# Kernel optimization log

Hardware: AMD Instinct MI355X
Metric: run time of the kernel (lower is better)

The kernel has to match this reference:

```python
import jax, jax.numpy as jnp
import numpy as np

EPS = 1e-8
N_REFINE = 10
LR_REFINE = 0.1
N_SAMPLES = 12
M_BLEND = 0.3      # self.m
MARGIN = 0.2
TAU = 0.07
USE_INFONCE = True


def safe_norm(x, axis=-1):
    return x / jnp.clip(jnp.linalg.norm(x, axis=axis, keepdims=True), EPS, None)


def setup_inputs() -> dict:
    key = jax.random.key(0)
    k1, k2, k3, k4 = jax.random.split(key, 4)
    K, C, N, H, W = 10, 768, 8, 64, 64
    fg_proto = safe_norm(jax.random.normal(k1, (K, C), jnp.float32))
    bg_proto = safe_norm(jax.random.normal(k2, (K, C), jnp.float32))
    F_map = jax.random.normal(k3, (N, C, H, W), jnp.float32)
    M_map = jax.random.uniform(k4, (N, 1, H, W), jnp.float32)
    return {"fg_proto": fg_proto, "bg_proto": bg_proto, "F_map": F_map, "M_map": M_map}


def _refine(feats, p0):
    """Iterative spherical k-means style refinement.
    feats: [S, C] unit vectors (constants), p0: [K, C] centers.
    Vectorized segment-sum version of the per-cluster torch loop
    (updates within one iteration are independent across k)."""
    K = p0.shape[0]
    ones = jnp.ones((feats.shape[0],), feats.dtype)

    def body(p, it):
        step = LR_REFINE / (1.0 + 0.5 * it)
        assign = jnp.argmax(feats @ p.T, axis=1)                      # [S]
        sums = jax.ops.segment_sum(feats, assign, num_segments=K)    # [K, C]
        cnts = jax.ops.segment_sum(ones, assign, num_segments=K)     # [K]
        mean = sums / jnp.clip(cnts, 1.0, None)[:, None]
        new = safe_norm((1.0 - step) * p + step * mean)
        p = jnp.where((cnts > 0)[:, None], new, p)
        return p, None

    p, _ = jax.lax.scan(body, p0, jnp.arange(N_REFINE, dtype=p0.dtype))
    return p


def reference(fg_proto, bg_proto, F_map, M_map):
    N, C, H, W = F_map.shape
    # mask already at feature resolution -> nearest interpolate is identity
    M_flat = jnp.clip(M_map, 0.0, 1.0).reshape(-1)                   # [N*H*W]
    F_flat = safe_norm(jnp.transpose(F_map, (0, 2, 3, 1)).reshape(-1, C))

    # min cosine distance to any prototype == 1 - max similarity
    dist_fg_min = 1.0 - jnp.max(F_flat @ fg_proto.T, axis=1)
    dist_bg_min = 1.0 - jnp.max(F_flat @ bg_proto.T, axis=1)
    score_fg = jax.lax.stop_gradient(dist_fg_min * M_flat)
    score_bg = jax.lax.stop_gradient(dist_bg_min * (1.0 - M_flat))
    pos_idx = jax.lax.top_k(score_fg, N_SAMPLES)[1]
    neg_idx = jax.lax.top_k(score_bg, N_SAMPLES)[1]

    pos_feats = F_flat[pos_idx]                                       # [12, C]
    neg_feats = F_flat[neg_idx]

    # refinement runs under torch.no_grad on detached copies
    p_fg = _refine(jax.lax.stop_gradient(pos_feats), jax.lax.stop_gradient(fg_proto))
    p_bg = _refine(jax.lax.stop_gradient(neg_feats), jax.lax.stop_gradient(bg_proto))

    # triplet loss
    pos_n = safe_norm(pos_feats)
    neg_n = safe_norm(neg_feats)
    sim_pos = jnp.mean(jnp.max(pos_n @ p_fg.T, axis=1))
    sim_neg = jnp.mean(jnp.max(neg_n @ p_fg.T, axis=1))
    loss = jax.nn.relu(MARGIN + sim_neg - sim_pos)

    if USE_INFONCE:
        pos_sim = pos_n @ p_fg.T / TAU                                # [12, K]
        neg_sim = pos_n @ p_bg.T / TAU                                # [12, K]
        numer = jax.nn.logsumexp(pos_sim, axis=1)
        denom = jax.nn.logsumexp(jnp.concatenate([pos_sim, neg_sim], axis=1), axis=1)
        loss = loss + 0.25 * (-jnp.mean(numer - denom))

    refined_fg = safe_norm((1.0 - M_BLEND) * fg_proto + M_BLEND * p_fg)
    refined_bg = safe_norm((1.0 - M_BLEND) * bg_proto + M_BLEND * p_bg)
    return loss, refined_fg, refined_bg
```

## Files before the change

### kernel.cpp

```cpp
#include <hip/hip_runtime.h>
#include <math.h>

#define KP   10
#define CC   768
#define NB   8
#define HW   4096
#define STOT 32768
#define NS   12
#define NBLK 256

#define WS_CAND  0
#define WS_FEATS 12352
#define WS_PFG   30784
#define WS_PBG   38464

typedef unsigned long long ull;
typedef float f2v __attribute__((ext_vector_type(2)));

__device__ __forceinline__ f2v fma2(f2v a, float b, f2v c) {
#if __has_builtin(__builtin_elementwise_fma)
    f2v bb = b;
    return __builtin_elementwise_fma(a, bb, c);
#else
    f2v r; r.x = fmaf(a.x, b, c.x); r.y = fmaf(a.y, b, c.y); return r;
#endif
}

__device__ __forceinline__ ull pack_key(float v, int idx) {
    unsigned u = __float_as_uint(v);
    u ^= (unsigned)((int)u >> 31) | 0x80000000u;
    return ((ull)u << 32) | (ull)(0xFFFFFFFFu - (unsigned)idx);
}

__global__ __launch_bounds__(1024) void k_scores(const float* __restrict__ fg,
                                                 const float* __restrict__ bg,
                                                 const float* __restrict__ F,
                                                 const float* __restrict__ M,
                                                 ull* __restrict__ cand) {
    __shared__ float pl[20 * CC];
    __shared__ float part[8][64][2][21];
    __shared__ ull kfl[128], kbl[128];

    const int tid  = threadIdx.x;
    const int w    = __builtin_amdgcn_readfirstlane(tid >> 6);
    const int lane = tid & 63;
    const int b    = blockIdx.x;
    const int n    = b >> 5;
    const int hwb  = (b & 31) * 128 + lane * 2;
    const float* fp = F + ((size_t)n * CC) * HW + hwb;
    const int cbase = w * 48;

    f2v fnA[8], fnB[8];
#pragma unroll
    for (int j = 0; j < 8; ++j)
        fnA[j] = __builtin_nontemporal_load((const f2v*)(fp + (size_t)(cbase + j) * HW));
#pragma unroll
    for (int j = 0; j < 8; ++j)
        fnB[j] = __builtin_nontemporal_load((const f2v*)(fp + (size_t)(cbase + 8 + j) * HW));

    for (int i = tid; i < KP * CC; i += 1024) {
        pl[i]           = fg[i];
        pl[KP * CC + i] = bg[i];
    }
    __syncthreads();

    f2v afg[KP], abg[KP], n2;
#pragma unroll
    for (int k = 0; k < KP; ++k) { afg[k] = 0.f; abg[k] = 0.f; }
    n2 = 0.f;

    for (int c0 = 0; c0 < 48; c0 += 8) {
        f2v f[8];
#pragma unroll
        for (int j = 0; j < 8; ++j) { f[j] = fnA[j]; fnA[j] = fnB[j]; }
        if (c0 + 16 < 48) {
#pragma unroll
            for (int j = 0; j < 8; ++j)
                fnB[j] = __builtin_nontemporal_load((const f2v*)(fp + (size_t)(cbase + c0 + 16 + j) * HW));
        }

#pragma unroll
        for (int k = 0; k < KP; ++k) {
            const float4* pq = (const float4*)&pl[k * CC + cbase + c0];
            float4 a = pq[0], c = pq[1];
            f2v acc = afg[k];
            acc = fma2(f[0], a.x, acc); acc = fma2(f[1], a.y, acc);
            acc = fma2(f[2], a.z, acc); acc = fma2(f[3], a.w, acc);
            acc = fma2(f[4], c.x, acc); acc = fma2(f[5], c.y, acc);
            acc = fma2(f[6], c.z, acc); acc = fma2(f[7], c.w, acc);
            afg[k] = acc;
        }
#pragma unroll
        for (int k = 0; k < KP; ++k) {
            const float4* pq = (const float4*)&pl[(KP + k) * CC + cbase + c0];
            float4 a = pq[0], c = pq[1];
            f2v acc = abg[k];
            acc = fma2(f[0], a.x, acc); acc = fma2(f[1], a.y, acc);
            acc = fma2(f[2], a.z, acc); acc = fma2(f[3], a.w, acc);
            acc = fma2(f[4], c.x, acc); acc = fma2(f[5], c.y, acc);
            acc = fma2(f[6], c.z, acc); acc = fma2(f[7], c.w, acc);
            abg[k] = acc;
        }
#pragma unroll
        for (int j = 0; j < 8; ++j) {
#if __has_builtin(__builtin_elementwise_fma)
            n2 = __builtin_elementwise_fma(f[j], f[j], n2);
#else
            n2.x = fmaf(f[j].x, f[j].x, n2.x); n2.y = fmaf(f[j].y, f[j].y, n2.y);
#endif
        }
    }

    if (w >= 8) {
#pragma unroll
        for (int k = 0; k < KP; ++k) {
            part[w - 8][lane][0][k]      = afg[k].x; part[w - 8][lane][1][k]      = afg[k].y;
            part[w - 8][lane][0][10 + k] = abg[k].x; part[w - 8][lane][1][10 + k] = abg[k].y;
        }
        part[w - 8][lane][0][20] = n2.x; part[w - 8][lane][1][20] = n2.y;
    }
    __syncthreads();
    if (w < 8) {
#pragma unroll
        for (int k = 0; k < KP; ++k) {
            part[w][lane][0][k]      += afg[k].x; part[w][lane][1][k]      += afg[k].y;
            part[w][lane][0][10 + k] += abg[k].x; part[w][lane][1][10 + k] += abg[k].y;
        }
        part[w][lane][0][20] += n2.x; part[w][lane][1][20] += n2.y;
    }
    __syncthreads();

    if (tid < 128) {
        const int lane2 = tid >> 1, j = tid & 1;
        float vals[21];
#pragma unroll
        for (int q = 0; q < 21; ++q) {
            float acc = 0.f;
#pragma unroll
            for (int ss = 0; ss < 8; ++ss) acc += part[ss][lane2][j][q];
            vals[q] = acc;
        }
        float mfg = vals[0], mbg = vals[10];
#pragma unroll
        for (int k = 1; k < KP; ++k) { mfg = fmaxf(mfg, vals[k]); mbg = fmaxf(mbg, vals[10 + k]); }
        float nc = fmaxf(sqrtf(vals[20]), 1e-8f);
        int sp = b * 128 + tid;
        float m = fminf(fmaxf(M[sp], 0.f), 1.f);
        kfl[tid] = pack_key((1.f - mfg / nc) * m, sp);
        kbl[tid] = pack_key((1.f - mbg / nc) * (1.f - m), sp);
    }
    __syncthreads();

    if (w == 0) {
        ull k0 = kfl[lane], k1 = kfl[64 + lane];
        for (int r = 0; r < NS; ++r) {
            ull bk = (k0 > k1) ? k0 : k1;
#pragma unroll
            for (int m2 = 1; m2 < 64; m2 <<= 1) {
                ull o = __shfl_xor(bk, m2, 64);
                bk = (o > bk) ? o : bk;
            }
            if (lane == 0) cand[b * NS + r] = bk;
            if (k0 == bk) k0 = 0ull;
            if (k1 == bk) k1 = 0ull;
        }
    } else if (w == 1) {
        ull k0 = kbl[lane], k1 = kbl[64 + lane];
        for (int r = 0; r < NS; ++r) {
            ull bk = (k0 > k1) ? k0 : k1;
#pragma unroll
            for (int m2 = 1; m2 < 64; m2 <<= 1) {
                ull o = __shfl_xor(bk, m2, 64);
                bk = (o > bk) ? o : bk;
            }
            if (lane == 0) cand[NBLK * NS + b * NS + r] = bk;
            if (k0 == bk) k0 = 0ull;
            if (k1 == bk) k1 = 0ull;
        }
    }
}

__global__ __launch_bounds__(1024) void k_refine_fused(const ull* __restrict__ cand,
                                                       const float* __restrict__ F,
                                                       const float* __restrict__ fg,
                                                       const float* __restrict__ bg,
                                                       float* __restrict__ pfg,
                                                       float* __restrict__ pbg,
                                                       float* __restrict__ feats,
                                                       float* __restrict__ out) {
    __shared__ float fe[NS * CC];
    __shared__ int   seli[NS];
    __shared__ float dots[NS][KP];
    __shared__ int   assign[NS];

    const int side = blockIdx.x;
    const int tid  = threadIdx.x;
    const int wave = __builtin_amdgcn_readfirstlane(tid >> 6);
    const int lane = tid & 63;
    const int k    = wave;
    const float* p0 = (side == 0) ? fg : bg;
    float* pout     = (side == 0) ? pfg : pbg;

    if (wave == 0) {
        const ull* cs = cand + side * (NBLK * NS);
        ull tv[NS];
#pragma unroll
        for (int q = 0; q < NS; ++q) tv[q] = 0ull;
        for (int c = 0; c < 48; ++c) {
            ull key = cs[c * 64 + lane];
            if (key > tv[NS - 1]) {
#pragma unroll
                for (int q = NS - 1; q >= 1; --q) {
                    bool shift = key > tv[q - 1];
                    bool here  = !shift && (key > tv[q]);
                    tv[q] = shift ? tv[q - 1] : (here ? key : tv[q]);
                }
                if (key > tv[0]) tv[0] = key;
            }
        }
        for (int r = 0; r < NS; ++r) {
            ull bk = tv[0];
#pragma unroll
            for (int m2 = 1; m2 < 64; m2 <<= 1) {
                ull o = __shfl_xor(bk, m2, 64);
                bk = (o > bk) ? o : bk;
            }
            if (lane == 0) seli[r] = (int)(0xFFFFFFFFu - (unsigned)(bk & 0xFFFFFFFFull));
            bool win = (tv[0] == bk);
#pragma unroll
            for (int q = 0; q < NS - 1; ++q) tv[q] = win ? tv[q + 1] : tv[q];
            tv[NS - 1] = win ? 0ull : tv[NS - 1];
        }
    }
    __syncthreads();

    for (int i = tid; i < NS * CC; i += 1024) {
        int srow = i / CC, c = i - srow * CC;
        int sp = seli[srow];
        int nn = sp >> 12, hh = sp & 4095;
        fe[i] = F[((size_t)nn * CC + c) * HW + hh];
    }
    __syncthreads();

    if (wave < NS) {
        float ssq = 0.f;
#pragma unroll
        for (int j = 0; j < 12; ++j) { float v = fe[wave * CC + j * 64 + lane]; ssq = fmaf(v, v, ssq); }
#pragma unroll
        for (int m2 = 1; m2 < 64; m2 <<= 1) ssq += __shfl_xor(ssq, m2, 64);
        float inv = 1.f / fmaxf(sqrtf(ssq), 1e-8f);
#pragma unroll
        for (int j = 0; j < 12; ++j) fe[wave * CC + j * 64 + lane] *= inv;
    }
    __syncthreads();

    {
        float4* fo = (float4*)(feats + side * (NS * CC));
        const float4* fi = (const float4*)fe;
        for (int i = tid; i < NS * CC / 4; i += 1024) fo[i] = fi[i];
    }

    float4 p[3];
#pragma unroll
    for (int j4 = 0; j4 < 3; ++j4) p[j4] = make_float4(0.f, 0.f, 0.f, 0.f);
    if (wave < KP) {
#pragma unroll
        for (int j4 = 0; j4 < 3; ++j4)
            p[j4] = *(const float4*)&p0[k * CC + j4 * 256 + lane * 4];
    }

    for (int it = 0; it < 10; ++it) {
        float step = 0.1f / (1.0f + 0.5f * (float)it);

        if (wave < KP) {
            float d[NS];
#pragma unroll
            for (int s = 0; s < NS; ++s) d[s] = 0.f;
#pragma unroll
            for (int j4 = 0; j4 < 3; ++j4) {
                float4 pv = p[j4];
#pragma unroll
                for (int s = 0; s < NS; ++s) {
                    float4 fv = *(const float4*)&fe[s * CC + j4 * 256 + lane * 4];
                    d[s] = fmaf(fv.x, pv.x, d[s]);
                    d[s] = fmaf(fv.y, pv.y, d[s]);
                    d[s] = fmaf(fv.z, pv.z, d[s]);
                    d[s] = fmaf(fv.w, pv.w, d[s]);
                }
            }
#pragma unroll
            for (int s = 0; s < NS; ++s) {
#pragma unroll
                for (int m2 = 1; m2 < 64; m2 <<= 1) d[s] += __shfl_xor(d[s], m2, 64);
            }
            if (lane == 0) {
#pragma unroll
                for (int s = 0; s < NS; ++s) dots[s][k] = d[s];
            }
        }
        __syncthreads();

        if (tid < NS) {
            float bv = dots[tid][0]; int bk = 0;
#pragma unroll
            for (int kk = 1; kk < KP; ++kk) { float v = dots[tid][kk]; if (v > bv) { bv = v; bk = kk; } }
            assign[tid] = bk;
        }
        __syncthreads();

        if (wave < KP) {
            int a[NS]; int cnt = 0;
#pragma unroll
            for (int s = 0; s < NS; ++s) { a[s] = assign[s]; cnt += (a[s] == k) ? 1 : 0; }

            if (cnt > 0) {
                float4 mac[3];
#pragma unroll
                for (int j4 = 0; j4 < 3; ++j4) mac[j4] = make_float4(0.f, 0.f, 0.f, 0.f);
#pragma unroll
                for (int s = 0; s < NS; ++s) {
                    if (a[s] == k) {
#pragma unroll
                        for (int j4 = 0; j4 < 3; ++j4) {
                            float4 fv = *(const float4*)&fe[s * CC + j4 * 256 + lane * 4];
                            mac[j4].x += fv.x; mac[j4].y += fv.y; mac[j4].z += fv.z; mac[j4].w += fv.w;
                        }
                    }
                }
                float fcnt = (float)cnt;
                float4 v[3]; float ss = 0.f;
#pragma unroll
                for (int j4 = 0; j4 < 3; ++j4) {
                    v[j4].x = (1.0f - step) * p[j4].x + step * (mac[j4].x / fcnt);
                    v[j4].y = (1.0f - step) * p[j4].y + step * (mac[j4].y / fcnt);
                    v[j4].z = (1.0f - step) * p[j4].z + step * (mac[j4].z / fcnt);
                    v[j4].w = (1.0f - step) * p[j4].w + step * (mac[j4].w / fcnt);
                    ss = fmaf(v[j4].x, v[j4].x, ss);
                    ss = fmaf(v[j4].y, v[j4].y, ss);
                    ss = fmaf(v[j4].z, v[j4].z, ss);
                    ss = fmaf(v[j4].w, v[j4].w, ss);
                }
#pragma unroll
                for (int m2 = 1; m2 < 64; m2 <<= 1) ss += __shfl_xor(ss, m2, 64);
                float inv = 1.f / fmaxf(sqrtf(ss), 1e-8f);
#pragma unroll
                for (int j4 = 0; j4 < 3; ++j4) {
                    p[j4].x = v[j4].x * inv; p[j4].y = v[j4].y * inv;
                    p[j4].z = v[j4].z * inv; p[j4].w = v[j4].w * inv;
                }
            }
        }
    }

    if (wave < KP) {
#pragma unroll
        for (int j4 = 0; j4 < 3; ++j4)
            *(float4*)&pout[k * CC + j4 * 256 + lane * 4] = p[j4];

        float4 vv[3]; float ss2 = 0.f;
#pragma unroll
        for (int j4 = 0; j4 < 3; ++j4) {
            float4 pz = *(const float4*)&p0[k * CC + j4 * 256 + lane * 4];
            vv[j4].x = 0.7f * pz.x + 0.3f * p[j4].x;
            vv[j4].y = 0.7f * pz.y + 0.3f * p[j4].y;
            vv[j4].z = 0.7f * pz.z + 0.3f * p[j4].z;
            vv[j4].w = 0.7f * pz.w + 0.3f * p[j4].w;
            ss2 = fmaf(vv[j4].x, vv[j4].x, ss2);
            ss2 = fmaf(vv[j4].y, vv[j4].y, ss2);
            ss2 = fmaf(vv[j4].z, vv[j4].z, ss2);
            ss2 = fmaf(vv[j4].w, vv[j4].w, ss2);
        }
#pragma unroll
        for (int m2 = 1; m2 < 64; m2 <<= 1) ss2 += __shfl_xor(ss2, m2, 64);
        float inv2 = 1.f / fmaxf(sqrtf(ss2), 1e-8f);
        float* orow = out + 1 + (side * KP + k) * CC;
#pragma unroll
        for (int j4 = 0; j4 < 3; ++j4) {
            float4 o4;
            o4.x = vv[j4].x * inv2; o4.y = vv[j4].y * inv2;
            o4.z = vv[j4].z * inv2; o4.w = vv[j4].w * inv2;
            *(float4*)&orow[j4 * 256 + lane * 4] = o4;
        }
    }
}

__global__ __launch_bounds__(1024) void k_loss(const float* __restrict__ feats,
                                               const float* __restrict__ pfg,
                                               const float* __restrict__ pbg,
                                               float* __restrict__ out) {
    __shared__ float dots3[NS * 30];
    __shared__ float mp[NS], mn[NS], infon[NS];
    int tid = threadIdx.x, wave = tid >> 6, lane = tid & 63;

    for (int pid = wave; pid < 360; pid += 16) {
        int g = pid / 120, rr = pid % 120, s = rr / KP, k = rr % KP;
        const float4* a4 = (const float4*)(feats + ((g == 1 ? NS + s : s) * CC) + lane * 12);
        const float4* b4 = (const float4*)((g == 2 ? pbg : pfg) + k * CC + lane * 12);
        float acc = 0.f;
#pragma unroll
        for (int j = 0; j < 3; ++j) {
            float4 a = a4[j], b = b4[j];
            acc += a.x * b.x + a.y * b.y + a.z * b.z + a.w * b.w;
        }
#pragma unroll
        for (int m2 = 1; m2 < 64; m2 <<= 1) acc += __shfl_xor(acc, m2, 64);
        if (lane == 0) dots3[s * 30 + g * 10 + k] = acc;
    }
    __syncthreads();

    if (tid < NS) {
        const float* d = &dots3[tid * 30];
        float maxp = d[0], maxn = d[10];
#pragma unroll
        for (int k = 1; k < KP; ++k) { maxp = fmaxf(maxp, d[k]); maxn = fmaxf(maxn, d[10 + k]); }
        mp[tid] = maxp; mn[tid] = maxn;

        float x[KP], y[KP];
#pragma unroll
        for (int k = 0; k < KP; ++k) { x[k] = d[k] / 0.07f; y[k] = d[20 + k] / 0.07f; }
        float m10 = x[0];
#pragma unroll
        for (int k = 1; k < KP; ++k) m10 = fmaxf(m10, x[k]);
        float se = 0.f;
#pragma unroll
        for (int k = 0; k < KP; ++k) se += expf(x[k] - m10);
        float numer = logf(se) + m10;
        float m20 = m10;
#pragma unroll
        for (int k = 0; k < KP; ++k) m20 = fmaxf(m20, y[k]);
        float se2 = 0.f;
#pragma unroll
        for (int k = 0; k < KP; ++k) se2 += expf(x[k] - m20);
#pragma unroll
        for (int k = 0; k < KP; ++k) se2 += expf(y[k] - m20);
        float denom = logf(se2) + m20;
        infon[tid] = numer - denom;
    }
    __syncthreads();
    if (tid == 0) {
        float sp = 0.f, sn = 0.f, si = 0.f;
        for (int s = 0; s < NS; ++s) { sp += mp[s]; sn += mn[s]; si += infon[s]; }
        sp /= 12.f; sn /= 12.f; si /= 12.f;
        float loss = fmaxf(0.2f + sn - sp, 0.f) + 0.25f * (-si);
        out[0] = loss;
    }
}

extern "C" void kernel_launch(void* const* d_in, const int* in_sizes, int n_in,
                              void* d_out, int out_size, void* d_ws, size_t ws_size,
                              hipStream_t stream) {
    const float* fg = (const float*)d_in[0];
    const float* bg = (const float*)d_in[1];
    const float* F  = (const float*)d_in[2];
    const float* M  = (const float*)d_in[3];
    float* out = (float*)d_out;

    float* w    = (float*)d_ws;
    ull*   cand = (ull*)(w + WS_CAND);
    float* fea  = w + WS_FEATS;
    float* pfg  = w + WS_PFG;
    float* pbg  = w + WS_PBG;

    k_scores      <<<NBLK, 1024, 0, stream>>>(fg, bg, F, M, cand);
    k_refine_fused<<<2, 1024, 0, stream>>>(cand, F, fg, bg, pfg, pbg, fea, out);
    k_loss        <<<1, 1024, 0, stream>>>(fea, pfg, pbg, out);
}
```

Baseline: 125.9 us.

## Run prototype refinement in Gram-matrix coefficient space inside one wave

Replaces the 10-iteration per-prototype refinement, which recomputed 768-wide dot products and needed two block barriers per iteration, with a closed form. Each prototype is a linear combination of its initial value and the 12 sample features. The kernel precomputes the sample-prototype dots, the sample Gram matrix and the prototype norms once, runs the iterations on scalars in a single wave, then rebuilds the final prototypes from the coefficients. It also stages the initial prototypes in shared memory. In exchange it adds extra shared memory and changes floating-point rounding order, which could flip near-tie argmax assignments.

```diff
diff --git a/kernel.cpp b/kernel.cpp
--- a/kernel.cpp
+++ b/kernel.cpp
@@ -189,17 +189,19 @@
                                                        float* __restrict__ feats,
                                                        float* __restrict__ out) {
     __shared__ float fe[NS * CC];
+    __shared__ float p0l[KP * CC];
     __shared__ int   seli[NS];
-    __shared__ float dots[NS][KP];
-    __shared__ int   assign[NS];
+    __shared__ float D0sh[NS * KP];
+    __shared__ float Gsh[NS * NS];
+    __shared__ float P2sh[KP];
+    __shared__ float coef[KP][13];
 
     const int side = blockIdx.x;
     const int tid  = threadIdx.x;
     const int wave = __builtin_amdgcn_readfirstlane(tid >> 6);
     const int lane = tid & 63;
-    const int k    = wave;
-    const float* p0 = (side == 0) ? fg : bg;
-    float* pout     = (side == 0) ? pfg : pbg;
+    const float* p0g = (side == 0) ? fg : bg;
+    float* pout      = (side == 0) ? pfg : pbg;
 
     if (wave == 0) {
         const ull* cs = cand + side * (NBLK * NS);
@@ -231,6 +233,8 @@
             for (int q = 0; q < NS - 1; ++q) tv[q] = win ? tv[q + 1] : tv[q];
             tv[NS - 1] = win ? 0ull : tv[NS - 1];
         }
+    } else {
+        for (int i = tid - 64; i < KP * CC; i += 960) p0l[i] = p0g[i];
     }
     __syncthreads();
 
@@ -260,115 +264,141 @@
         for (int i = tid; i < NS * CC / 4; i += 1024) fo[i] = fi[i];
     }
 
-    float4 p[3];
-#pragma unroll
-    for (int j4 = 0; j4 < 3; ++j4) p[j4] = make_float4(0.f, 0.f, 0.f, 0.f);
+    for (int t = wave; t < 274; t += 16) {
+        const float *A, *B; float* dst;
+        if (t < 120)      { int s = t / 10, k = t - 10 * s; A = &fe[s * CC];  B = &p0l[k * CC]; dst = &D0sh[t]; }
+        else if (t < 264) { int u = t - 120; int s = u / 12, s2 = u - 12 * s; A = &fe[s * CC]; B = &fe[s2 * CC]; dst = &Gsh[u]; }
+        else              { int k = t - 264; A = &p0l[k * CC]; B = A; dst = &P2sh[k]; }
+        const float4* A4 = (const float4*)A;
+        const float4* B4 = (const float4*)B;
+        float acc = 0.f;
+#pragma unroll
+        for (int j4 = 0; j4 < 3; ++j4) {
+            float4 a = A4[j4 * 64 + lane], b = B4[j4 * 64 + lane];
+            acc = fmaf(a.x, b.x, acc); acc = fmaf(a.y, b.y, acc);
+            acc = fmaf(a.z, b.z, acc); acc = fmaf(a.w, b.w, acc);
+        }
+#pragma unroll
+        for (int m2 = 1; m2 < 64; m2 <<= 1) acc += __shfl_xor(acc, m2, 64);
+        if (lane == 0) *dst = acc;
+    }
+    __syncthreads();
+
+    if (wave == 0) {
+        float d[KP], g[NS], p2[KP];
+#pragma unroll
+        for (int k = 0; k < KP; ++k) d[k] = (lane < NS) ? D0sh[lane * KP + k] : 0.f;
+#pragma unroll
+        for (int s = 0; s < NS; ++s) g[s] = (lane < NS) ? Gsh[lane * NS + s] : 0.f;
+#pragma unroll
+        for (int k = 0; k < KP; ++k) p2[k] = P2sh[k];
+        float alpha = 1.f, beta[NS];
+#pragma unroll
+        for (int s = 0; s < NS; ++s) beta[s] = 0.f;
+
+        for (int it = 0; it < 10; ++it) {
+            float step = 0.1f / (1.0f + 0.5f * (float)it);
+            float om = 1.0f - step;
+
+            int aL = 0; float bv = d[0];
+#pragma unroll
+            for (int k = 1; k < KP; ++k) { if (d[k] > bv) { bv = d[k]; aL = k; } }
+
+            int av[NS]; float vv[NS];
+#pragma unroll
+            for (int s = 0; s < NS; ++s) { av[s] = __shfl(aL, s, 64); vv[s] = __shfl(bv, s, 64); }
+
+            float T[KP]; float W = 0.f;
+#pragma unroll
+            for (int k = 0; k < KP; ++k) {
+                float t = 0.f;
+#pragma unroll
+                for (int s = 0; s < NS; ++s) t += (av[s] == k) ? g[s] : 0.f;
+                T[k] = t;
+                if (k == aL) W = t;
+            }
+            float wv[NS];
+#pragma unroll
+            for (int s = 0; s < NS; ++s) wv[s] = __shfl(W, s, 64);
+
+            float mynorm = 1.f, mysc = 0.f; int mycnt = 0;
+#pragma unroll
+            for (int k = 0; k < KP; ++k) {
+                int c = 0; float S1 = 0.f, U = 0.f;
+#pragma unroll
+                for (int s = 0; s < NS; ++s) {
+                    bool m = (av[s] == k);
+                    c += m ? 1 : 0;
+                    S1 += m ? vv[s] : 0.f;
+                    U  += m ? wv[s] : 0.f;
+                }
+                if (c > 0) {
+                    float sc = step / (float)c;
+                    float nv = om * om * p2[k] + 2.f * om * sc * S1 + sc * sc * U;
+                    float nrm = fmaxf(sqrtf(fmaxf(nv, 0.f)), 1e-8f);
+                    float inv = 1.f / nrm;
+                    d[k] = (om * d[k] + sc * T[k]) * inv;
+                    p2[k] = 1.f;
+                    if (k == lane) { mynorm = inv; mysc = sc; mycnt = c; }
+                }
+            }
+
+            if (lane < KP && mycnt > 0) {
+                alpha *= om * mynorm;
+#pragma unroll
+                for (int s = 0; s < NS; ++s)
+                    beta[s] = (om * beta[s] + ((av[s] == lane) ? mysc : 0.f)) * mynorm;
+            }
+        }
+
+        if (lane < KP) {
+            coef[lane][0] = alpha;
+#pragma unroll
+            for (int s = 0; s < NS; ++s) coef[lane][1 + s] = beta[s];
+        }
+    }
+    __syncthreads();
+
     if (wave < KP) {
-#pragma unroll
-        for (int j4 = 0; j4 < 3; ++j4)
-            p[j4] = *(const float4*)&p0[k * CC + j4 * 256 + lane * 4];
-    }
-
-    for (int it = 0; it < 10; ++it) {
-        float step = 0.1f / (1.0f + 0.5f * (float)it);
-
-        if (wave < KP) {
-            float d[NS];
-#pragma unroll
-            for (int s = 0; s < NS; ++s) d[s] = 0.f;
-#pragma unroll
-            for (int j4 = 0; j4 < 3; ++j4) {
-                float4 pv = p[j4];
-#pragma unroll
-                for (int s = 0; s < NS; ++s) {
-                    float4 fv = *(const float4*)&fe[s * CC + j4 * 256 + lane * 4];
-                    d[s] = fmaf(fv.x, pv.x, d[s]);
-                    d[s] = fmaf(fv.y, pv.y, d[s]);
-                    d[s] = fmaf(fv.z, pv.z, d[s]);
-                    d[s] = fmaf(fv.w, pv.w, d[s]);
-                }
-            }
+        const int k = wave;
+        float alpha = coef[k][0];
+        float bt[NS];
+#pragma unroll
+        for (int s = 0; s < NS; ++s) bt[s] = coef[k][1 + s];
+
+        float4 p[3];
+#pragma unroll
+        for (int j4 = 0; j4 < 3; ++j4) {
+            float4 a = *(const float4*)&p0l[k * CC + j4 * 256 + lane * 4];
+            float4 acc;
+            acc.x = alpha * a.x; acc.y = alpha * a.y; acc.z = alpha * a.z; acc.w = alpha * a.w;
 #pragma unroll
             for (int s = 0; s < NS; ++s) {
-#pragma unroll
-                for (int m2 = 1; m2 < 64; m2 <<= 1) d[s] += __shfl_xor(d[s], m2, 64);
-            }
-            if (lane == 0) {
-#pragma unroll
-                for (int s = 0; s < NS; ++s) dots[s][k] = d[s];
-            }
-        }
-        __syncthreads();
-
-        if (tid < NS) {
-            float bv = dots[tid][0]; int bk = 0;
-#pragma unroll
-            for (int kk = 1; kk < KP; ++kk) { float v = dots[tid][kk]; if (v > bv) { bv = v; bk = kk; } }
-            assign[tid] = bk;
-        }
-        __syncthreads();
-
-        if (wave < KP) {
-            int a[NS]; int cnt = 0;
-#pragma unroll
-            for (int s = 0; s < NS; ++s) { a[s] = assign[s]; cnt += (a[s] == k) ? 1 : 0; }
-
-            if (cnt > 0) {
-                float4 mac[3];
-#pragma unroll
-                for (int j4 = 0; j4 < 3; ++j4) mac[j4] = make_float4(0.f, 0.f, 0.f, 0.f);
-#pragma unroll
-                for (int s = 0; s < NS; ++s) {
-                    if (a[s] == k) {
-#pragma unroll
-                        for (int j4 = 0; j4 < 3; ++j4) {
-                            float4 fv = *(const float4*)&fe[s * CC + j4 * 256 + lane * 4];
-                            mac[j4].x += fv.x; mac[j4].y += fv.y; mac[j4].z += fv.z; mac[j4].w += fv.w;
-                        }
-                    }
-                }
-                float fcnt = (float)cnt;
-                float4 v[3]; float ss = 0.f;
-#pragma unroll
-                for (int j4 = 0; j4 < 3; ++j4) {
-                    v[j4].x = (1.0f - step) * p[j4].x + step * (mac[j4].x / fcnt);
-                    v[j4].y = (1.0f - step) * p[j4].y + step * (mac[j4].y / fcnt);
-                    v[j4].z = (1.0f - step) * p[j4].z + step * (mac[j4].z / fcnt);
-                    v[j4].w = (1.0f - step) * p[j4].w + step * (mac[j4].w / fcnt);
-                    ss = fmaf(v[j4].x, v[j4].x, ss);
-                    ss = fmaf(v[j4].y, v[j4].y, ss);
-                    ss = fmaf(v[j4].z, v[j4].z, ss);
-                    ss = fmaf(v[j4].w, v[j4].w, ss);
-                }
-#pragma unroll
-                for (int m2 = 1; m2 < 64; m2 <<= 1) ss += __shfl_xor(ss, m2, 64);
-                float inv = 1.f / fmaxf(sqrtf(ss), 1e-8f);
-#pragma unroll
-                for (int j4 = 0; j4 < 3; ++j4) {
-                    p[j4].x = v[j4].x * inv; p[j4].y = v[j4].y * inv;
-                    p[j4].z = v[j4].z * inv; p[j4].w = v[j4].w * inv;
-                }
-            }
-        }
-    }
-
-    if (wave < KP) {
+                float4 fv = *(const float4*)&fe[s * CC + j4 * 256 + lane * 4];
+                acc.x = fmaf(bt[s], fv.x, acc.x);
+                acc.y = fmaf(bt[s], fv.y, acc.y);
+                acc.z = fmaf(bt[s], fv.z, acc.z);
+                acc.w = fmaf(bt[s], fv.w, acc.w);
+            }
+            p[j4] = acc;
+        }
+
 #pragma unroll
         for (int j4 = 0; j4 < 3; ++j4)
             *(float4*)&pout[k * CC + j4 * 256 + lane * 4] = p[j4];
 
-        float4 vv[3]; float ss2 = 0.f;
+        float4 vv4[3]; float ss2 = 0.f;
 #pragma unroll
         for (int j4 = 0; j4 < 3; ++j4) {
-            float4 pz = *(const float4*)&p0[k * CC + j4 * 256 + lane * 4];
-            vv[j4].x = 0.7f * pz.x + 0.3f * p[j4].x;
-            vv[j4].y = 0.7f * pz.y + 0.3f * p[j4].y;
-            vv[j4].z = 0.7f * pz.z + 0.3f * p[j4].z;
-            vv[j4].w = 0.7f * pz.w + 0.3f * p[j4].w;
-            ss2 = fmaf(vv[j4].x, vv[j4].x, ss2);
-            ss2 = fmaf(vv[j4].y, vv[j4].y, ss2);
-            ss2 = fmaf(vv[j4].z, vv[j4].z, ss2);
-            ss2 = fmaf(vv[j4].w, vv[j4].w, ss2);
+            float4 pz = *(const float4*)&p0l[k * CC + j4 * 256 + lane * 4];
+            vv4[j4].x = 0.7f * pz.x + 0.3f * p[j4].x;
+            vv4[j4].y = 0.7f * pz.y + 0.3f * p[j4].y;
+            vv4[j4].z = 0.7f * pz.z + 0.3f * p[j4].z;
+            vv4[j4].w = 0.7f * pz.w + 0.3f * p[j4].w;
+            ss2 = fmaf(vv4[j4].x, vv4[j4].x, ss2);
+            ss2 = fmaf(vv4[j4].y, vv4[j4].y, ss2);
+            ss2 = fmaf(vv4[j4].z, vv4[j4].z, ss2);
+            ss2 = fmaf(vv4[j4].w, vv4[j4].w, ss2);
         }
 #pragma unroll
         for (int m2 = 1; m2 < 64; m2 <<= 1) ss2 += __shfl_xor(ss2, m2, 64);
@@ -377,8 +407,8 @@
 #pragma unroll
         for (int j4 = 0; j4 < 3; ++j4) {
             float4 o4;
-            o4.x = vv[j4].x * inv2; o4.y = vv[j4].y * inv2;
-            o4.z = vv[j4].z * inv2; o4.w = vv[j4].w * inv2;
+            o4.x = vv4[j4].x * inv2; o4.y = vv4[j4].y * inv2;
+            o4.z = vv4[j4].z * inv2; o4.w = vv4[j4].w * inv2;
             *(float4*)&orow[j4 * 256 + lane * 4] = o4;
         }
     }
```

Result: slower. 137.2 us (+9.0%).

## Fuse refinement and loss into a single-block tail kernel using shared memory

Applied to the files above, without the earlier changes.

Merges the two-block refinement kernel and the single-block loss kernel into one block that refines both fg and bg prototypes together, keeping normalized features and refined prototypes in LDS instead of round-tripping through global workspace. This removes one kernel launch and the global stores and reloads between the stages. In exchange, the two sides' refinements now run serially inside one workgroup rather than in parallel on two CUs, which roughly doubles per-wave work and register pressure in the refinement loop. LDS use also grows to about 135KB.

```diff
diff --git a/kernel.cpp b/kernel.cpp
--- a/kernel.cpp
+++ b/kernel.cpp
@@ -10,9 +10,6 @@
 #define NBLK 256
 
 #define WS_CAND  0
-#define WS_FEATS 12352
-#define WS_PFG   30784
-#define WS_PBG   38464
 
 typedef unsigned long long ull;
 typedef float f2v __attribute__((ext_vector_type(2)));
@@ -180,29 +177,25 @@
     }
 }
 
-__global__ __launch_bounds__(1024) void k_refine_fused(const ull* __restrict__ cand,
-                                                       const float* __restrict__ F,
-                                                       const float* __restrict__ fg,
-                                                       const float* __restrict__ bg,
-                                                       float* __restrict__ pfg,
-                                                       float* __restrict__ pbg,
-                                                       float* __restrict__ feats,
-                                                       float* __restrict__ out) {
-    __shared__ float fe[NS * CC];
-    __shared__ int   seli[NS];
-    __shared__ float dots[NS][KP];
-    __shared__ int   assign[NS];
-
-    const int side = blockIdx.x;
+__global__ __launch_bounds__(1024) void k_tail(const ull* __restrict__ cand,
+                                               const float* __restrict__ F,
+                                               const float* __restrict__ fg,
+                                               const float* __restrict__ bg,
+                                               float* __restrict__ out) {
+    __shared__ float fe[2 * NS * CC];
+    __shared__ float pl[2 * KP * CC];
+    __shared__ int   seli[2 * NS];
+    __shared__ float dots[2][NS][KP];
+    __shared__ int   assign[2][NS];
+    __shared__ float dots3[NS * 30];
+    __shared__ float mp[NS], mn[NS], infon[NS];
+
     const int tid  = threadIdx.x;
-    const int wave = __builtin_amdgcn_readfirstlane(tid >> 6);
+    const int w    = __builtin_amdgcn_readfirstlane(tid >> 6);
     const int lane = tid & 63;
-    const int k    = wave;
-    const float* p0 = (side == 0) ? fg : bg;
-    float* pout     = (side == 0) ? pfg : pbg;
-
-    if (wave == 0) {
-        const ull* cs = cand + side * (NBLK * NS);
+
+    if (w < 2) {
+        const ull* cs = cand + w * (NBLK * NS);
         ull tv[NS];
 #pragma unroll
         for (int q = 0; q < NS; ++q) tv[q] = 0ull;
@@ -225,186 +218,193 @@
                 ull o = __shfl_xor(bk, m2, 64);
                 bk = (o > bk) ? o : bk;
             }
-            if (lane == 0) seli[r] = (int)(0xFFFFFFFFu - (unsigned)(bk & 0xFFFFFFFFull));
+            if (lane == 0) seli[w * NS + r] = (int)(0xFFFFFFFFu - (unsigned)(bk & 0xFFFFFFFFull));
             bool win = (tv[0] == bk);
 #pragma unroll
             for (int q = 0; q < NS - 1; ++q) tv[q] = win ? tv[q + 1] : tv[q];
             tv[NS - 1] = win ? 0ull : tv[NS - 1];
         }
-    }
-    __syncthreads();
-
-    for (int i = tid; i < NS * CC; i += 1024) {
-        int srow = i / CC, c = i - srow * CC;
-        int sp = seli[srow];
-        int nn = sp >> 12, hh = sp & 4095;
-        fe[i] = F[((size_t)nn * CC + c) * HW + hh];
-    }
-    __syncthreads();
-
-    if (wave < NS) {
+    } else {
+        for (int i = tid - 128; i < 2 * KP * CC; i += 896)
+            pl[i] = (i < KP * CC) ? fg[i] : bg[i - KP * CC];
+    }
+    __syncthreads();
+
+    for (int i = tid; i < 2 * NS * CC; i += 1024) {
+        int row = i / CC, c = i - row * CC;
+        int sp = seli[row];
+        fe[i] = F[((size_t)(sp >> 12) * CC + c) * HW + (sp & 4095)];
+    }
+    __syncthreads();
+
+    for (int row = w; row < 2 * NS; row += 16) {
         float ssq = 0.f;
 #pragma unroll
-        for (int j = 0; j < 12; ++j) { float v = fe[wave * CC + j * 64 + lane]; ssq = fmaf(v, v, ssq); }
+        for (int j = 0; j < 12; ++j) { float v = fe[row * CC + j * 64 + lane]; ssq = fmaf(v, v, ssq); }
 #pragma unroll
         for (int m2 = 1; m2 < 64; m2 <<= 1) ssq += __shfl_xor(ssq, m2, 64);
         float inv = 1.f / fmaxf(sqrtf(ssq), 1e-8f);
 #pragma unroll
-        for (int j = 0; j < 12; ++j) fe[wave * CC + j * 64 + lane] *= inv;
-    }
-    __syncthreads();
-
-    {
-        float4* fo = (float4*)(feats + side * (NS * CC));
-        const float4* fi = (const float4*)fe;
-        for (int i = tid; i < NS * CC / 4; i += 1024) fo[i] = fi[i];
-    }
-
-    float4 p[3];
-#pragma unroll
-    for (int j4 = 0; j4 < 3; ++j4) p[j4] = make_float4(0.f, 0.f, 0.f, 0.f);
-    if (wave < KP) {
-#pragma unroll
-        for (int j4 = 0; j4 < 3; ++j4)
-            p[j4] = *(const float4*)&p0[k * CC + j4 * 256 + lane * 4];
+        for (int j = 0; j < 12; ++j) fe[row * CC + j * 64 + lane] *= inv;
+    }
+    __syncthreads();
+
+    float4 p[2][3];
+#pragma unroll
+    for (int sd = 0; sd < 2; ++sd)
+#pragma unroll
+        for (int j4 = 0; j4 < 3; ++j4) p[sd][j4] = make_float4(0.f, 0.f, 0.f, 0.f);
+    if (w < KP) {
+#pragma unroll
+        for (int sd = 0; sd < 2; ++sd)
+#pragma unroll
+            for (int j4 = 0; j4 < 3; ++j4)
+                p[sd][j4] = *(const float4*)&pl[(sd * KP + w) * CC + j4 * 256 + lane * 4];
     }
 
     for (int it = 0; it < 10; ++it) {
         float step = 0.1f / (1.0f + 0.5f * (float)it);
 
-        if (wave < KP) {
-            float d[NS];
-#pragma unroll
-            for (int s = 0; s < NS; ++s) d[s] = 0.f;
-#pragma unroll
-            for (int j4 = 0; j4 < 3; ++j4) {
-                float4 pv = p[j4];
+        if (w < KP) {
+            float d[2][NS];
+#pragma unroll
+            for (int sd = 0; sd < 2; ++sd)
+#pragma unroll
+                for (int s = 0; s < NS; ++s) d[sd][s] = 0.f;
+#pragma unroll
+            for (int sd = 0; sd < 2; ++sd) {
+#pragma unroll
+                for (int j4 = 0; j4 < 3; ++j4) {
+                    float4 pv = p[sd][j4];
+#pragma unroll
+                    for (int s = 0; s < NS; ++s) {
+                        float4 fv = *(const float4*)&fe[(sd * NS + s) * CC + j4 * 256 + lane * 4];
+                        d[sd][s] = fmaf(fv.x, pv.x, d[sd][s]);
+                        d[sd][s] = fmaf(fv.y, pv.y, d[sd][s]);
+                        d[sd][s] = fmaf(fv.z, pv.z, d[sd][s]);
+                        d[sd][s] = fmaf(fv.w, pv.w, d[sd][s]);
+                    }
+                }
+            }
+#pragma unroll
+            for (int sd = 0; sd < 2; ++sd)
 #pragma unroll
                 for (int s = 0; s < NS; ++s) {
-                    float4 fv = *(const float4*)&fe[s * CC + j4 * 256 + lane * 4];
-                    d[s] = fmaf(fv.x, pv.x, d[s]);
-                    d[s] = fmaf(fv.y, pv.y, d[s]);
-                    d[s] = fmaf(fv.z, pv.z, d[s]);
-                    d[s] = fmaf(fv.w, pv.w, d[s]);
+#pragma unroll
+                    for (int m2 = 1; m2 < 64; m2 <<= 1) d[sd][s] += __shfl_xor(d[sd][s], m2, 64);
                 }
-            }
-#pragma unroll
-            for (int s = 0; s < NS; ++s) {
-#pragma unroll
-                for (int m2 = 1; m2 < 64; m2 <<= 1) d[s] += __shfl_xor(d[s], m2, 64);
-            }
             if (lane == 0) {
 #pragma unroll
-                for (int s = 0; s < NS; ++s) dots[s][k] = d[s];
+                for (int sd = 0; sd < 2; ++sd)
+#pragma unroll
+                    for (int s = 0; s < NS; ++s) dots[sd][s][w] = d[sd][s];
             }
         }
         __syncthreads();
 
-        if (tid < NS) {
-            float bv = dots[tid][0]; int bk = 0;
-#pragma unroll
-            for (int kk = 1; kk < KP; ++kk) { float v = dots[tid][kk]; if (v > bv) { bv = v; bk = kk; } }
-            assign[tid] = bk;
+        if (tid < 2 * NS) {
+            int sd = tid / NS, s = tid - sd * NS;
+            float bv = dots[sd][s][0]; int bk = 0;
+#pragma unroll
+            for (int kk = 1; kk < KP; ++kk) { float v = dots[sd][s][kk]; if (v > bv) { bv = v; bk = kk; } }
+            assign[sd][s] = bk;
         }
         __syncthreads();
 
-        if (wave < KP) {
-            int a[NS]; int cnt = 0;
-#pragma unroll
-            for (int s = 0; s < NS; ++s) { a[s] = assign[s]; cnt += (a[s] == k) ? 1 : 0; }
-
-            if (cnt > 0) {
-                float4 mac[3];
-#pragma unroll
-                for (int j4 = 0; j4 < 3; ++j4) mac[j4] = make_float4(0.f, 0.f, 0.f, 0.f);
-#pragma unroll
-                for (int s = 0; s < NS; ++s) {
-                    if (a[s] == k) {
-#pragma unroll
-                        for (int j4 = 0; j4 < 3; ++j4) {
-                            float4 fv = *(const float4*)&fe[s * CC + j4 * 256 + lane * 4];
-                            mac[j4].x += fv.x; mac[j4].y += fv.y; mac[j4].z += fv.z; mac[j4].w += fv.w;
+        if (w < KP) {
+#pragma unroll
+            for (int sd = 0; sd < 2; ++sd) {
+                int a[NS]; int cnt = 0;
+#pragma unroll
+                for (int s = 0; s < NS; ++s) { a[s] = assign[sd][s]; cnt += (a[s] == w) ? 1 : 0; }
+                if (cnt > 0) {
+                    float4 mac[3];
+#pragma unroll
+                    for (int j4 = 0; j4 < 3; ++j4) mac[j4] = make_float4(0.f, 0.f, 0.f, 0.f);
+#pragma unroll
+                    for (int s = 0; s < NS; ++s) {
+                        if (a[s] == w) {
+#pragma unroll
+                            for (int j4 = 0; j4 < 3; ++j4) {
+                                float4 fv = *(const float4*)&fe[(sd * NS + s) * CC + j4 * 256 + lane * 4];
+                                mac[j4].x += fv.x; mac[j4].y += fv.y; mac[j4].z += fv.z; mac[j4].w += fv.w;
+                            }
                         }
                     }
+                    float fcnt = (float)cnt;
+                    float4 v[3]; float ss = 0.f;
+#pragma unroll
+                    for (int j4 = 0; j4 < 3; ++j4) {
+                        v[j4].x = (1.0f - step) * p[sd][j4].x + step * (mac[j4].x / fcnt);
+                        v[j4].y = (1.0f - step) * p[sd][j4].y + step * (mac[j4].y / fcnt);
+                        v[j4].z = (1.0f - step) * p[sd][j4].z + step * (mac[j4].z / fcnt);
+                        v[j4].w = (1.0f - step) * p[sd][j4].w + step * (mac[j4].w / fcnt);
+                        ss = fmaf(v[j4].x, v[j4].x, ss);
+                        ss = fmaf(v[j4].y, v[j4].y, ss);
+                        ss = fmaf(v[j4].z, v[j4].z, ss);
+                        ss = fmaf(v[j4].w, v[j4].w, ss);
+                    }
+#pragma unroll
+                    for (int m2 = 1; m2 < 64; m2 <<= 1) ss += __shfl_xor(ss, m2, 64);
+                    float inv = 1.f / fmaxf(sqrtf(ss), 1e-8f);
+#pragma unroll
+                    for (int j4 = 0; j4 < 3; ++j4) {
+                        p[sd][j4].x = v[j4].x * inv; p[sd][j4].y = v[j4].y * inv;
+                        p[sd][j4].z = v[j4].z * inv; p[sd][j4].w = v[j4].w * inv;
+                    }
                 }
-                float fcnt = (float)cnt;
-                float4 v[3]; float ss = 0.f;
-#pragma unroll
-                for (int j4 = 0; j4 < 3; ++j4) {
-                    v[j4].x = (1.0f - step) * p[j4].x + step * (mac[j4].x / fcnt);
-                    v[j4].y = (1.0f - step) * p[j4].y + step * (mac[j4].y / fcnt);
-                    v[j4].z = (1.0f - step) * p[j4].z + step * (mac[j4].z / fcnt);
-                    v[j4].w = (1.0f - step) * p[j4].w + step * (mac[j4].w / fcnt);
-                    ss = fmaf(v[j4].x, v[j4].x, ss);
-                    ss = fmaf(v[j4].y, v[j4].y, ss);
-                    ss = fmaf(v[j4].z, v[j4].z, ss);
-                    ss = fmaf(v[j4].w, v[j4].w, ss);
-                }
-#pragma unroll
-                for (int m2 = 1; m2 < 64; m2 <<= 1) ss += __shfl_xor(ss, m2, 64);
-                float inv = 1.f / fmaxf(sqrtf(ss), 1e-8f);
-#pragma unroll
-                for (int j4 = 0; j4 < 3; ++j4) {
-                    p[j4].x = v[j4].x * inv; p[j4].y = v[j4].y * inv;
-                    p[j4].z = v[j4].z * inv; p[j4].w = v[j4].w * inv;
-                }
-            }
-        }
-    }
-
-    if (wave < KP) {
-#pragma unroll
-        for (int j4 = 0; j4 < 3; ++j4)
-            *(float4*)&pout[k * CC + j4 * 256 + lane * 4] = p[j4];
-
-        float4 vv[3]; float ss2 = 0.f;
+            }
+        }
+    }
+
+    if (w < KP) {
+#pragma unroll
+        for (int sd = 0; sd < 2; ++sd) {
+            float* prow = &pl[(sd * KP + w) * CC];
+            float4 vv[3]; float ss2 = 0.f;
+#pragma unroll
+            for (int j4 = 0; j4 < 3; ++j4) {
+                float4 pz = *(const float4*)&prow[j4 * 256 + lane * 4];
+                vv[j4].x = 0.7f * pz.x + 0.3f * p[sd][j4].x;
+                vv[j4].y = 0.7f * pz.y + 0.3f * p[sd][j4].y;
+                vv[j4].z = 0.7f * pz.z + 0.3f * p[sd][j4].z;
+                vv[j4].w = 0.7f * pz.w + 0.3f * p[sd][j4].w;
+                ss2 = fmaf(vv[j4].x, vv[j4].x, ss2);
+                ss2 = fmaf(vv[j4].y, vv[j4].y, ss2);
+                ss2 = fmaf(vv[j4].z, vv[j4].z, ss2);
+                ss2 = fmaf(vv[j4].w, vv[j4].w, ss2);
+            }
+#pragma unroll
+            for (int m2 = 1; m2 < 64; m2 <<= 1) ss2 += __shfl_xor(ss2, m2, 64);
+            float inv2 = 1.f / fmaxf(sqrtf(ss2), 1e-8f);
+            float* orow = out + 1 + (sd * KP + w) * CC;
+#pragma unroll
+            for (int j4 = 0; j4 < 3; ++j4) {
+                float4 o4;
+                o4.x = vv[j4].x * inv2; o4.y = vv[j4].y * inv2;
+                o4.z = vv[j4].z * inv2; o4.w = vv[j4].w * inv2;
+                *(float4*)&orow[j4 * 256 + lane * 4] = o4;
+                *(float4*)&prow[j4 * 256 + lane * 4] = p[sd][j4];
+            }
+        }
+    }
+    __syncthreads();
+
+    for (int pid = w; pid < 360; pid += 16) {
+        int g = pid / 120, rr = pid % 120, s = rr / KP, kk = rr % KP;
+        const float* A = &fe[((g == 1 ? NS : 0) + s) * CC];
+        const float* B = &pl[((g == 2 ? KP : 0) + kk) * CC];
+        float acc = 0.f;
 #pragma unroll
         for (int j4 = 0; j4 < 3; ++j4) {
-            float4 pz = *(const float4*)&p0[k * CC + j4 * 256 + lane * 4];
-            vv[j4].x = 0.7f * pz.x + 0.3f * p[j4].x;
-            vv[j4].y = 0.7f * pz.y + 0.3f * p[j4].y;
-            vv[j4].z = 0.7f * pz.z + 0.3f * p[j4].z;
-            vv[j4].w = 0.7f * pz.w + 0.3f * p[j4].w;
-            ss2 = fmaf(vv[j4].x, vv[j4].x, ss2);
-            ss2 = fmaf(vv[j4].y, vv[j4].y, ss2);
-            ss2 = fmaf(vv[j4].z, vv[j4].z, ss2);
-            ss2 = fmaf(vv[j4].w, vv[j4].w, ss2);
-        }
-#pragma unroll
-        for (int m2 = 1; m2 < 64; m2 <<= 1) ss2 += __shfl_xor(ss2, m2, 64);
-        float inv2 = 1.f / fmaxf(sqrtf(ss2), 1e-8f);
-        float* orow = out + 1 + (side * KP + k) * CC;
-#pragma unroll
-        for (int j4 = 0; j4 < 3; ++j4) {
-            float4 o4;
-            o4.x = vv[j4].x * inv2; o4.y = vv[j4].y * inv2;
-            o4.z = vv[j4].z * inv2; o4.w = vv[j4].w * inv2;
-            *(float4*)&orow[j4 * 256 + lane * 4] = o4;
-        }
-    }
-}
-
-__global__ __launch_bounds__(1024) void k_loss(const float* __restrict__ feats,
-                                               const float* __restrict__ pfg,
-                                               const float* __restrict__ pbg,
-                                               float* __restrict__ out) {
-    __shared__ float dots3[NS * 30];
-    __shared__ float mp[NS], mn[NS], infon[NS];
-    int tid = threadIdx.x, wave = tid >> 6, lane = tid & 63;
-
-    for (int pid = wave; pid < 360; pid += 16) {
-        int g = pid / 120, rr = pid % 120, s = rr / KP, k = rr % KP;
-        const float4* a4 = (const float4*)(feats + ((g == 1 ? NS + s : s) * CC) + lane * 12);
-        const float4* b4 = (const float4*)((g == 2 ? pbg : pfg) + k * CC + lane * 12);
-        float acc = 0.f;
-#pragma unroll
-        for (int j = 0; j < 3; ++j) {
-            float4 a = a4[j], b = b4[j];
-            acc += a.x * b.x + a.y * b.y + a.z * b.z + a.w * b.w;
+            float4 a = *(const float4*)&A[j4 * 256 + lane * 4];
+            float4 b = *(const float4*)&B[j4 * 256 + lane * 4];
+            acc = fmaf(a.x, b.x, acc); acc = fmaf(a.y, b.y, acc);
+            acc = fmaf(a.z, b.z, acc); acc = fmaf(a.w, b.w, acc);
         }
 #pragma unroll
         for (int m2 = 1; m2 < 64; m2 <<= 1) acc += __shfl_xor(acc, m2, 64);
-        if (lane == 0) dots3[s * 30 + g * 10 + k] = acc;
+        if (lane == 0) dots3[s * 30 + g * 10 + kk] = acc;
     }
     __syncthreads();
 
@@ -455,13 +455,8 @@
     const float* M  = (const float*)d_in[3];
     float* out = (float*)d_out;
 
-    float* w    = (float*)d_ws;
-    ull*   cand = (ull*)(w + WS_CAND);
-    float* fea  = w + WS_FEATS;
-    float* pfg  = w + WS_PFG;
-    float* pbg  = w + WS_PBG;
-
-    k_scores      <<<NBLK, 1024, 0, stream>>>(fg, bg, F, M, cand);
-    k_refine_fused<<<2, 1024, 0, stream>>>(cand, F, fg, bg, pfg, pbg, fea, out);
-    k_loss        <<<1, 1024, 0, stream>>>(fea, pfg, pbg, out);
+    ull* cand = (ull*)((float*)d_ws + WS_CAND);
+
+    k_scores<<<NBLK, 1024, 0, stream>>>(fg, bg, F, M, cand);
+    k_tail  <<<1, 1024, 0, stream>>>(cand, F, fg, bg, out);
 }
```

After: 176.3 us. +40.1%, slower.
